# Kernel optimization log

Hardware: AMD Instinct MI355X
Metric: run time of the kernel (lower is better)

## Reference

```python
import math
import jax, jax.numpy as jnp
import numpy as np

N_HEAD = 8
SEQ_LEN = 2048
D_MODEL = 2048  # must equal SEQ_LEN for the original module to run


def setup_inputs() -> dict:
    key = jax.random.key(0)
    ks = jax.random.split(key, 8)
    # xavier-normal-ish init scale for [S, S] weights
    std = math.sqrt(2.0 / (SEQ_LEN + SEQ_LEN))
    def w(k):
        return jax.random.normal(k, (SEQ_LEN, SEQ_LEN), dtype=jnp.float32) * std
    x = jax.random.normal(ks[0], (N_HEAD * SEQ_LEN, D_MODEL), dtype=jnp.float32)
    return {
        "x": x,
        "Wq1": w(ks[1]), "Wk1": w(ks[2]),
        "Wq2": w(ks[3]), "Wk2": w(ks[4]),
        "Wv": w(ks[5]), "W1": w(ks[6]), "W2": w(ks[7]),
    }


def reference(x, Wq1, Wk1, Wq2, Wk2, Wv, W1, W2):
    # x: [n_head*S, D] -> [n_head, S, D]; nn.Linear(W) computes y = x @ W.T
    rx = x.reshape(N_HEAD, SEQ_LEN, D_MODEL)
    scale = 1.0 / math.sqrt(SEQ_LEN)

    q1 = jnp.einsum('hsd,ed->hse', rx, Wq1)
    k1 = jnp.einsum('hsd,ed->hse', rx, Wk1)
    q2 = jnp.einsum('hsd,ed->hse', rx, Wq2)
    k2 = jnp.einsum('hsd,ed->hse', rx, Wk2)
    v = jnp.einsum('hsd,ed->hse', rx, Wv)

    a1 = jax.nn.softmax(jnp.einsum('hse,hte->hst', q1, k1) * scale, axis=-1)
    a2 = jax.nn.softmax(jnp.einsum('hse,hte->hst', q2, k2) * scale, axis=-1)
    score1 = jnp.einsum('hst,ut->hsu', a1, W1)
    score2 = jnp.einsum('hst,ut->hsu', a2, W2)

    diff = score1 - score2
    circle = diff * diff  # [h, S, S]
    return jnp.einsum('hst,htd->hsd', circle, v)
```

## Files before the change

kernel.cpp:

```cpp
#include <hip/hip_runtime.h>
#include <math.h>

typedef unsigned short u16;
typedef __bf16 bf16x8 __attribute__((ext_vector_type(8)));
typedef float floatx4 __attribute__((ext_vector_type(4)));

__device__ __forceinline__ u16 f2bf(float f) {
    unsigned int u = __float_as_uint(f);
    u += 0x7FFFu + ((u >> 16) & 1u);
    return (u16)(u >> 16);
}

__device__ __forceinline__ void async_load16(const void* g, void* l) {
    __builtin_amdgcn_global_load_lds(
        (const __attribute__((address_space(1))) unsigned int*)g,
        (__attribute__((address_space(3))) unsigned int*)l, 16, 0, 0);
}

#define BM 128
#define BN 128
#define BK 32

template<int OUT_BF16, int EPI>
__global__ __launch_bounds__(256)
void gemm_mfma(const u16* __restrict__ A, const u16* __restrict__ B,
               void* __restrict__ Cv, const float* __restrict__ E,
               int N, int K,
               long long sA, long long sB, long long sC, long long sE)
{
    __shared__ u16 As[2][BM * BK];
    __shared__ u16 Bs[2][BN * BK];

    const long long z = blockIdx.z;
    A += z * sA;
    B += z * sB;

    const int gx = gridDim.x;
    const int nwg = gx * gridDim.y;
    int wg = blockIdx.y * gx + blockIdx.x;
    if ((nwg & 7) == 0) wg = (wg & 7) * (nwg >> 3) + (wg >> 3);
    const int bx = wg % gx, by = wg / gx;

    const int tid  = threadIdx.x;
    const int w    = tid >> 6;
    const int lane = tid & 63;

    const int srow = w * 16 + (lane >> 2);
    const int skp  = ((lane & 3) ^ ((lane >> 3) & 3)) * 8;
    const u16* Ag = A + ((long long)by * BM + srow) * K + skp;
    const u16* Bg = B + ((long long)bx * BN + srow) * K + skp;
    const long long rstep = (long long)64 * K;
    const int lds_off = w * 512 + lane * 8;

    const int wm   = (w >> 1) * 64, wn = (w & 1) * 64;
    const int frow = lane & 15, quad = lane >> 4;
    const int rsw  = (frow >> 1) & 3;
    const int slot = (quad ^ rsw) * 8;

    floatx4 acc[4][4];
#pragma unroll
    for (int i = 0; i < 4; i++)
#pragma unroll
        for (int j = 0; j < 4; j++) acc[i][j] = (floatx4)0.0f;

    const int NT = K / BK;

    async_load16(Ag,         &As[0][lds_off]);
    async_load16(Ag + rstep, &As[0][lds_off + 64 * BK]);
    async_load16(Bg,         &Bs[0][lds_off]);
    async_load16(Bg + rstep, &Bs[0][lds_off + 64 * BK]);
    __syncthreads();

    for (int t = 0; t < NT; ++t) {
        const int cur = t & 1;
        if (t + 1 < NT) {
            const long long ko = (long long)(t + 1) * BK;
            async_load16(Ag + ko,         &As[cur ^ 1][lds_off]);
            async_load16(Ag + ko + rstep, &As[cur ^ 1][lds_off + 64 * BK]);
            async_load16(Bg + ko,         &Bs[cur ^ 1][lds_off]);
            async_load16(Bg + ko + rstep, &Bs[cur ^ 1][lds_off + 64 * BK]);
        }

        union { int4 i4; bf16x8 v; } a[4], b[4];
#pragma unroll
        for (int i = 0; i < 4; i++)
            a[i].i4 = *(const int4*)&As[cur][(wm + 16 * i + frow) * BK + slot];
#pragma unroll
        for (int j = 0; j < 4; j++)
            b[j].i4 = *(const int4*)&Bs[cur][(wn + 16 * j + frow) * BK + slot];
#pragma unroll
        for (int i = 0; i < 4; i++)
#pragma unroll
            for (int j = 0; j < 4; j++)
                acc[i][j] = __builtin_amdgcn_mfma_f32_16x16x32_bf16(
                    a[i].v, b[j].v, acc[i][j], 0, 0, 0);

        __syncthreads();
    }

    const long long crow0 = (long long)by * BM + wm + quad * 4;
    const long long ccol0 = (long long)bx * BN + wn + frow;
    u16*   Cb = (u16*)Cv   + z * sC;
    float* Cf = (float*)Cv + z * sC;
    const float* Ep = EPI ? (E + z * sE) : nullptr;
#pragma unroll
    for (int i = 0; i < 4; i++) {
#pragma unroll
        for (int r = 0; r < 4; r++) {
            const long long gr = crow0 + 16 * i + r;
#pragma unroll
            for (int j = 0; j < 4; j++) {
                const long long gc = ccol0 + 16 * j;
                float v = acc[i][j][r];
                if (EPI) {
                    const float e = Ep[gr * (long long)N + gc];
                    const float d = e - v;
                    v = d * d;
                }
                if (OUT_BF16) Cb[gr * (long long)N + gc] = f2bf(v);
                else          Cf[gr * (long long)N + gc] = v;
            }
        }
    }
}

__global__ __launch_bounds__(256)
void softmax_bf16(const float* __restrict__ P, u16* __restrict__ O, float scale)
{
    const long long rb = (long long)blockIdx.x * 2048;
    const float* p = P + rb;
    const int tid = threadIdx.x;

    const float4 x0 = *(const float4*)(p + tid * 8);
    const float4 x1 = *(const float4*)(p + tid * 8 + 4);
    float v[8] = {x0.x, x0.y, x0.z, x0.w, x1.x, x1.y, x1.z, x1.w};

    float m = -1e30f;
#pragma unroll
    for (int j = 0; j < 8; j++) { v[j] *= scale; m = fmaxf(m, v[j]); }
#pragma unroll
    for (int off = 32; off; off >>= 1) m = fmaxf(m, __shfl_xor(m, off));

    __shared__ float smax[4];
    __shared__ float ssum[4];
    const int wid = tid >> 6, lane = tid & 63;
    if (lane == 0) smax[wid] = m;
    __syncthreads();
    m = fmaxf(fmaxf(smax[0], smax[1]), fmaxf(smax[2], smax[3]));

    float s = 0.f;
#pragma unroll
    for (int j = 0; j < 8; j++) { v[j] = __expf(v[j] - m); s += v[j]; }
#pragma unroll
    for (int off = 32; off; off >>= 1) s += __shfl_xor(s, off);
    if (lane == 0) ssum[wid] = s;
    __syncthreads();
    const float inv = 1.f / (ssum[0] + ssum[1] + ssum[2] + ssum[3]);

    unsigned int p0 = f2bf(v[0] * inv) | ((unsigned int)f2bf(v[1] * inv) << 16);
    unsigned int p1 = f2bf(v[2] * inv) | ((unsigned int)f2bf(v[3] * inv) << 16);
    unsigned int p2 = f2bf(v[4] * inv) | ((unsigned int)f2bf(v[5] * inv) << 16);
    unsigned int p3 = f2bf(v[6] * inv) | ((unsigned int)f2bf(v[7] * inv) << 16);
    *(uint4*)(O + rb + tid * 8) = make_uint4(p0, p1, p2, p3);
}

__global__ __launch_bounds__(256)
void cast_bf16(const float* __restrict__ S, u16* __restrict__ D)
{
    const long long i = ((long long)blockIdx.x * 256 + threadIdx.x) * 8;
    const float4 a = *(const float4*)(S + i);
    const float4 b = *(const float4*)(S + i + 4);
    unsigned int p0 = f2bf(a.x) | ((unsigned int)f2bf(a.y) << 16);
    unsigned int p1 = f2bf(a.z) | ((unsigned int)f2bf(a.w) << 16);
    unsigned int p2 = f2bf(b.x) | ((unsigned int)f2bf(b.y) << 16);
    unsigned int p3 = f2bf(b.z) | ((unsigned int)f2bf(b.w) << 16);
    *(uint4*)(D + i) = make_uint4(p0, p1, p2, p3);
}

extern "C" void kernel_launch(void* const* d_in, const int* in_sizes, int n_in,
                              void* d_out, int out_size, void* d_ws, size_t ws_size,
                              hipStream_t stream)
{
    const float* x   = (const float*)d_in[0];
    const float* Wq1 = (const float*)d_in[1];
    const float* Wk1 = (const float*)d_in[2];
    const float* Wq2 = (const float*)d_in[3];
    const float* Wk2 = (const float*)d_in[4];
    const float* Wv  = (const float*)d_in[5];
    const float* W1  = (const float*)d_in[6];
    const float* W2  = (const float*)d_in[7];
    float* out = (float*)d_out;

    const int S = 2048, D = 2048;
    const int MS = 8 * S;
    const long long SS = (long long)S * S;
    const long long SD = (long long)S * D;

    u16* xb  = (u16*)d_ws;
    u16* wb  = xb + (size_t)MS * D;
    u16* wq1 = wb + 0 * SS; u16* wk1 = wb + 1 * SS;
    u16* wq2 = wb + 2 * SS; u16* wk2 = wb + 3 * SS;
    u16* wv  = wb + 4 * SS; u16* w1  = wb + 5 * SS; u16* w2 = wb + 6 * SS;
    u16* Qb  = wb + 7 * SS;
    u16* Kb  = Qb + (size_t)MS * D;
    float* Ab = (float*)(Kb + (size_t)MS * D);
    float* S1 = Ab + (size_t)MS * D;
    u16* Pb = Qb;
    u16* Cb = (u16*)Ab;
    u16* Vt = Kb;

    const float scale = 1.0f / sqrtf((float)S);

    dim3 blk(256);
    dim3 gFull(D / BN, MS / BM, 1);
    dim3 gHead(S / BN, S / BM, 8);
    dim3 gSm(MS);

    cast_bf16<<<dim3((MS * (long long)D) / 2048), blk, 0, stream>>>(x, xb);
    cast_bf16<<<dim3(SS / 2048), blk, 0, stream>>>(Wq1, wq1);
    cast_bf16<<<dim3(SS / 2048), blk, 0, stream>>>(Wk1, wk1);
    cast_bf16<<<dim3(SS / 2048), blk, 0, stream>>>(Wq2, wq2);
    cast_bf16<<<dim3(SS / 2048), blk, 0, stream>>>(Wk2, wk2);
    cast_bf16<<<dim3(SS / 2048), blk, 0, stream>>>(Wv, wv);
    cast_bf16<<<dim3(SS / 2048), blk, 0, stream>>>(W1, w1);
    cast_bf16<<<dim3(SS / 2048), blk, 0, stream>>>(W2, w2);

    gemm_mfma<1,0><<<gFull, blk, 0, stream>>>(xb, wq1, Qb, nullptr, D, D, 0, 0, 0, 0);
    gemm_mfma<1,0><<<gFull, blk, 0, stream>>>(xb, wk1, Kb, nullptr, D, D, 0, 0, 0, 0);
    gemm_mfma<0,0><<<gHead, blk, 0, stream>>>(Qb, Kb, Ab, nullptr, S, D, SS, SS, SS, 0);
    softmax_bf16<<<gSm, blk, 0, stream>>>(Ab, Pb, scale);
    gemm_mfma<0,0><<<gFull, blk, 0, stream>>>(Pb, w1, S1, nullptr, S, S, 0, 0, 0, 0);

    gemm_mfma<1,0><<<gFull, blk, 0, stream>>>(xb, wq2, Qb, nullptr, D, D, 0, 0, 0, 0);
    gemm_mfma<1,0><<<gFull, blk, 0, stream>>>(xb, wk2, Kb, nullptr, D, D, 0, 0, 0, 0);
    gemm_mfma<0,0><<<gHead, blk, 0, stream>>>(Qb, Kb, Ab, nullptr, S, D, SS, SS, SS, 0);
    softmax_bf16<<<gSm, blk, 0, stream>>>(Ab, Pb, scale);
    gemm_mfma<1,1><<<gFull, blk, 0, stream>>>(Pb, w2, Cb, S1, S, S, 0, 0, 0, 0);

    gemm_mfma<1,0><<<gHead, blk, 0, stream>>>(wv, xb, Vt, nullptr, S, D, 0, SD, SS, 0);
    gemm_mfma<0,0><<<gHead, blk, 0, stream>>>(Cb, Vt, out, nullptr, D, S, SS, SS, SD, 0);
}
```

Before: 2.078 ms.

## Enlarge GEMM tiles to 256x256x64 with 8 waves and finer-grained async pipelining

The MFMA GEMM moves from 128x128x32 tiles with 4 waves to 256x256x64 tiles with 8 waves per block. Each wave now holds 8x4 accumulator fragments. The main loop is split into four phases that interleave LDS fragment reads, async global-to-LDS loads for the next A tile and the B tile two steps ahead, explicit vmcnt/lgkmcnt waits, barriers and s_setprio around MFMA bursts. The aim is more data reuse per LDS byte and better overlap of memory with compute. The cost is much higher register pressure, 64 KB of LDS per block, fewer blocks in the grid, and a fragile hand-tuned synchronisation scheme.

```diff
diff --git a/kernel.cpp b/kernel.cpp
--- a/kernel.cpp
+++ b/kernel.cpp
@@ -17,19 +17,26 @@
         (__attribute__((address_space(3))) unsigned int*)l, 16, 0, 0);
 }
 
-#define BM 128
-#define BN 128
-#define BK 32
+#define BM 256
+#define BN 256
+#define BK 64
+#define TILE (BM * BK)
+
+#define BAR()        __builtin_amdgcn_s_barrier()
+#define WAIT_LGKM0() do { asm volatile("s_waitcnt lgkmcnt(0)" ::: "memory"); \
+                          __builtin_amdgcn_sched_barrier(0); } while (0)
+#define WAIT_VM(N)   do { asm volatile("s_waitcnt vmcnt(" #N ")" ::: "memory"); \
+                          __builtin_amdgcn_sched_barrier(0); } while (0)
 
 template<int OUT_BF16, int EPI>
-__global__ __launch_bounds__(256)
+__global__ __launch_bounds__(512, 2)
 void gemm_mfma(const u16* __restrict__ A, const u16* __restrict__ B,
                void* __restrict__ Cv, const float* __restrict__ E,
                int N, int K,
                long long sA, long long sB, long long sC, long long sE)
 {
-    __shared__ u16 As[2][BM * BK];
-    __shared__ u16 Bs[2][BN * BK];
+    __shared__ u16 As[2 * TILE];
+    __shared__ u16 Bs[2 * TILE];
 
     const long long z = blockIdx.z;
     A += z * sA;
@@ -45,80 +52,125 @@
     const int w    = tid >> 6;
     const int lane = tid & 63;
 
-    const int srow = w * 16 + (lane >> 2);
-    const int skp  = ((lane & 3) ^ ((lane >> 3) & 3)) * 8;
-    const u16* Ag = A + ((long long)by * BM + srow) * K + skp;
-    const u16* Bg = B + ((long long)bx * BN + srow) * K + skp;
-    const long long rstep = (long long)64 * K;
-    const int lds_off = w * 512 + lane * 8;
-
-    const int wm   = (w >> 1) * 64, wn = (w & 1) * 64;
+    const int srow = (w << 3) + (lane >> 3);
+    const int skc  = (lane & 7) ^ (lane >> 3);
+    const u16* Ag = A + ((long long)by * BM + srow) * K + skc * 8;
+    const u16* Bg = B + ((long long)bx * BN + srow) * K + skc * 8;
+    u16* AsS = As + srow * BK + (lane & 7) * 8;
+    u16* BsS = Bs + srow * BK + (lane & 7) * 8;
+    const long long rK64  = (long long)64 * K;
+    const long long rK128 = (long long)128 * K;
+
+    auto stageA = [&](int buf, int t, int h) {
+        const u16* g = Ag + (long long)h * rK128 + (long long)t * BK;
+        u16* l = AsS + buf * TILE + h * (128 * BK);
+        async_load16(g, l);
+        async_load16(g + rK64, l + 64 * BK);
+    };
+    auto stageB = [&](int buf, int t, int h) {
+        const u16* g = Bg + (long long)h * rK128 + (long long)t * BK;
+        u16* l = BsS + buf * TILE + h * (128 * BK);
+        async_load16(g, l);
+        async_load16(g + rK64, l + 64 * BK);
+    };
+
+    const int wrow = w >> 2, wcol = w & 3;
     const int frow = lane & 15, quad = lane >> 4;
-    const int rsw  = (frow >> 1) & 3;
-    const int slot = (quad ^ rsw) * 8;
-
-    floatx4 acc[4][4];
-#pragma unroll
-    for (int i = 0; i < 4; i++)
+    const int sw0  = ((quad ^ (frow & 7)) << 3);
+    const int aoff = (wrow * 128 + frow) * BK;
+    const int boff = (wcol * 64  + frow) * BK;
+
+    floatx4 acc[8][4];
+#pragma unroll
+    for (int i = 0; i < 8; i++)
 #pragma unroll
         for (int j = 0; j < 4; j++) acc[i][j] = (floatx4)0.0f;
 
     const int NT = K / BK;
 
-    async_load16(Ag,         &As[0][lds_off]);
-    async_load16(Ag + rstep, &As[0][lds_off + 64 * BK]);
-    async_load16(Bg,         &Bs[0][lds_off]);
-    async_load16(Bg + rstep, &Bs[0][lds_off + 64 * BK]);
-    __syncthreads();
+    stageA(0, 0, 0); stageA(0, 0, 1);
+    stageB(0, 0, 0); stageB(0, 0, 1);
+    if (NT > 1) {
+        stageB(1, 1, 0); stageB(1, 1, 1);
+        WAIT_VM(4);
+    } else {
+        WAIT_VM(0);
+    }
+    BAR();
+
+    union F { int4 i4; bf16x8 v; };
 
     for (int t = 0; t < NT; ++t) {
-        const int cur = t & 1;
-        if (t + 1 < NT) {
-            const long long ko = (long long)(t + 1) * BK;
-            async_load16(Ag + ko,         &As[cur ^ 1][lds_off]);
-            async_load16(Ag + ko + rstep, &As[cur ^ 1][lds_off + 64 * BK]);
-            async_load16(Bg + ko,         &Bs[cur ^ 1][lds_off]);
-            async_load16(Bg + ko + rstep, &Bs[cur ^ 1][lds_off + 64 * BK]);
+        const int b = t & 1;
+        const int abase = b * TILE + aoff;
+        const int bbase = b * TILE + boff;
+        const bool t1ok = (t + 1 < NT);
+        const bool t2ok = (t + 2 < NT);
+        F bfr[4][2];
+
+#pragma unroll
+        for (int q = 0; q < 4; ++q) {
+            if (q == 0) {
+#pragma unroll
+                for (int j = 0; j < 4; ++j) {
+                    bfr[j][0].i4 = *(const int4*)&Bs[bbase + j * (16 * BK) + sw0];
+                    bfr[j][1].i4 = *(const int4*)&Bs[bbase + j * (16 * BK) + (sw0 ^ 32)];
+                }
+            }
+            F af[2][2];
+#pragma unroll
+            for (int ii = 0; ii < 2; ++ii) {
+                const int ro = abase + (2 * q + ii) * (16 * BK);
+                af[ii][0].i4 = *(const int4*)&As[ro + sw0];
+                af[ii][1].i4 = *(const int4*)&As[ro + (sw0 ^ 32)];
+            }
+            if (q == 0 && t1ok) stageA(b ^ 1, t + 1, 0);
+            if (q == 1 && t1ok) stageA(b ^ 1, t + 1, 1);
+            if (q == 2 && t2ok) stageB(b,     t + 2, 0);
+            if (q == 3 && t2ok) stageB(b,     t + 2, 1);
+
+            BAR();
+            WAIT_LGKM0();
+            __builtin_amdgcn_s_setprio(1);
+#pragma unroll
+            for (int kk = 0; kk < 2; ++kk)
+#pragma unroll
+                for (int ii = 0; ii < 2; ++ii)
+#pragma unroll
+                    for (int j = 0; j < 4; ++j)
+                        acc[2 * q + ii][j] = __builtin_amdgcn_mfma_f32_16x16x32_bf16(
+                            af[ii][kk].v, bfr[j][kk].v, acc[2 * q + ii][j], 0, 0, 0);
+            __builtin_amdgcn_s_setprio(0);
+
+            if (q == 3) {
+                if (t2ok) { WAIT_VM(4); } else { WAIT_VM(0); }
+            }
+            BAR();
         }
-
-        union { int4 i4; bf16x8 v; } a[4], b[4];
-#pragma unroll
-        for (int i = 0; i < 4; i++)
-            a[i].i4 = *(const int4*)&As[cur][(wm + 16 * i + frow) * BK + slot];
-#pragma unroll
-        for (int j = 0; j < 4; j++)
-            b[j].i4 = *(const int4*)&Bs[cur][(wn + 16 * j + frow) * BK + slot];
-#pragma unroll
-        for (int i = 0; i < 4; i++)
-#pragma unroll
-            for (int j = 0; j < 4; j++)
-                acc[i][j] = __builtin_amdgcn_mfma_f32_16x16x32_bf16(
-                    a[i].v, b[j].v, acc[i][j], 0, 0, 0);
-
-        __syncthreads();
     }
 
-    const long long crow0 = (long long)by * BM + wm + quad * 4;
-    const long long ccol0 = (long long)bx * BN + wn + frow;
+    const long long crow0 = (long long)by * BM + wrow * 128 + quad * 4;
+    const long long ccol0 = (long long)bx * BN + wcol * 64 + frow;
     u16*   Cb = (u16*)Cv   + z * sC;
     float* Cf = (float*)Cv + z * sC;
     const float* Ep = EPI ? (E + z * sE) : nullptr;
 #pragma unroll
-    for (int i = 0; i < 4; i++) {
-#pragma unroll
-        for (int r = 0; r < 4; r++) {
+    for (int i = 0; i < 8; ++i) {
+#pragma unroll
+        for (int r = 0; r < 4; ++r) {
             const long long gr = crow0 + 16 * i + r;
-#pragma unroll
-            for (int j = 0; j < 4; j++) {
+            const long long rb = gr * (long long)N;
+#pragma unroll
+            for (int j = 0; j < 4; ++j) {
                 const long long gc = ccol0 + 16 * j;
                 float v = acc[i][j][r];
                 if (EPI) {
-                    const float e = Ep[gr * (long long)N + gc];
+                    const float e = Ep[rb + gc];
                     const float d = e - v;
                     v = d * d;
                 }
-                if (OUT_BF16) Cb[gr * (long long)N + gc] = f2bf(v);
-                else          Cf[gr * (long long)N + gc] = v;
+                if (OUT_BF16) Cb[rb + gc] = f2bf(v);
+                else          Cf[rb + gc] = v;
             }
         }
     }
@@ -212,6 +264,7 @@
     const float scale = 1.0f / sqrtf((float)S);
 
     dim3 blk(256);
+    dim3 blkG(512);
     dim3 gFull(D / BN, MS / BM, 1);
     dim3 gHead(S / BN, S / BM, 8);
     dim3 gSm(MS);
@@ -225,18 +278,18 @@
     cast_bf16<<<dim3(SS / 2048), blk, 0, stream>>>(W1, w1);
     cast_bf16<<<dim3(SS / 2048), blk, 0, stream>>>(W2, w2);
 
-    gemm_mfma<1,0><<<gFull, blk, 0, stream>>>(xb, wq1, Qb, nullptr, D, D, 0, 0, 0, 0);
-    gemm_mfma<1,0><<<gFull, blk, 0, stream>>>(xb, wk1, Kb, nullptr, D, D, 0, 0, 0, 0);
-    gemm_mfma<0,0><<<gHead, blk, 0, stream>>>(Qb, Kb, Ab, nullptr, S, D, SS, SS, SS, 0);
+    gemm_mfma<1,0><<<gFull, blkG, 0, stream>>>(xb, wq1, Qb, nullptr, D, D, 0, 0, 0, 0);
+    gemm_mfma<1,0><<<gFull, blkG, 0, stream>>>(xb, wk1, Kb, nullptr, D, D, 0, 0, 0, 0);
+    gemm_mfma<0,0><<<gHead, blkG, 0, stream>>>(Qb, Kb, Ab, nullptr, S, D, SS, SS, SS, 0);
     softmax_bf16<<<gSm, blk, 0, stream>>>(Ab, Pb, scale);
-    gemm_mfma<0,0><<<gFull, blk, 0, stream>>>(Pb, w1, S1, nullptr, S, S, 0, 0, 0, 0);
-
-    gemm_mfma<1,0><<<gFull, blk, 0, stream>>>(xb, wq2, Qb, nullptr, D, D, 0, 0, 0, 0);
-    gemm_mfma<1,0><<<gFull, blk, 0, stream>>>(xb, wk2, Kb, nullptr, D, D, 0, 0, 0, 0);
-    gemm_mfma<0,0><<<gHead, blk, 0, stream>>>(Qb, Kb, Ab, nullptr, S, D, SS, SS, SS, 0);
+    gemm_mfma<0,0><<<gFull, blkG, 0, stream>>>(Pb, w1, S1, nullptr, S, S, 0, 0, 0, 0);
+
+    gemm_mfma<1,0><<<gFull, blkG, 0, stream>>>(xb, wq2, Qb, nullptr, D, D, 0, 0, 0, 0);
+    gemm_mfma<1,0><<<gFull, blkG, 0, stream>>>(xb, wk2, Kb, nullptr, D, D, 0, 0, 0, 0);
+    gemm_mfma<0,0><<<gHead, blkG, 0, stream>>>(Qb, Kb, Ab, nullptr, S, D, SS, SS, SS, 0);
     softmax_bf16<<<gSm, blk, 0, stream>>>(Ab, Pb, scale);
-    gemm_mfma<1,1><<<gFull, blk, 0, stream>>>(Pb, w2, Cb, S1, S, S, 0, 0, 0, 0);
-
-    gemm_mfma<1,0><<<gHead, blk, 0, stream>>>(wv, xb, Vt, nullptr, S, D, 0, SD, SS, 0);
-    gemm_mfma<0,0><<<gHead, blk, 0, stream>>>(Cb, Vt, out, nullptr, D, S, SS, SS, SD, 0);
-}
+    gemm_mfma<1,1><<<gFull, blkG, 0, stream>>>(Pb, w2, Cb, S1, S, S, 0, 0, 0, 0);
+
+    gemm_mfma<1,0><<<gHead, blkG, 0, stream>>>(wv, xb, Vt, nullptr, S, D, 0, SD, SS, 0);
+    gemm_mfma<0,0><<<gHead, blkG, 0, stream>>>(Cb, Vt, out, nullptr, D, S, SS, SS, SD, 0);
+}
```

After: 1.840 ms. 1.13x faster.
